# Optimization experiments

Measured on AMD Instinct MI355X. Metric: run time of the kernel, lower is better.

The kernel has to match this reference:

```python
import jax, jax.numpy as jnp
import numpy as np
from jax import lax

WIN = 5
EPS = 1e-08
SHAPE = (2, 1, 160, 192, 224)


def _box1d(x, axis, win):
    """Sliding-window sum of size `win` along `axis`, zero-padded (same size).
    Uses a cumsum difference -> O(1) work per voxel instead of dense conv."""
    pad = win // 2
    pw = [(0, 0)] * x.ndim
    pw[axis] = (pad + 1, pad)
    c = jnp.cumsum(jnp.pad(x, pw), axis=axis)
    n = x.shape[axis]
    hi = lax.slice_in_dim(c, win, win + n, axis=axis)
    lo = lax.slice_in_dim(c, 0, n, axis=axis)
    return hi - lo


def _box_sum3d(x, win):
    for axis in (2, 3, 4):
        x = _box1d(x, axis, win)
    return x


def setup_inputs() -> dict:
    key = jax.random.key(0)
    k1, k2, k3 = jax.random.split(key, 3)
    I = jax.random.uniform(k1, SHAPE, dtype=jnp.float32)
    J = jax.random.uniform(k2, SHAPE, dtype=jnp.float32)
    weight_map = jax.random.uniform(k3, SHAPE, dtype=jnp.float32)
    return {"I": I, "J": J, "weight_map": weight_map}


def reference(I, J, weight_map):
    win = WIN
    win_size = float(win ** 3)
    I_sum = _box_sum3d(I, win)
    J_sum = _box_sum3d(J, win)
    I2_sum = _box_sum3d(I * I, win)
    J2_sum = _box_sum3d(J * J, win)
    IJ_sum = _box_sum3d(I * J, win)
    u_I = I_sum / win_size
    u_J = J_sum / win_size
    cross = IJ_sum - u_J * I_sum - u_I * J_sum + u_I * u_J * win_size
    I_var = I2_sum - 2.0 * u_I * I_sum + u_I * u_I * win_size
    J_var = J2_sum - 2.0 * u_J * J_sum + u_J * u_J * win_size
    cc = cross * cross / (I_var * J_var + EPS)
    return -1.0 * jnp.mean(cc * weight_map)
```

## Files before the change

### kernel.cpp

```cpp
#include <hip/hip_runtime.h>

#define N_  2
#define D_  160
#define H_  192
#define W_  224
#define TW  32
#define TH  16
#define ZCH 20
#define NZC (D_/ZCH)
#define HR  (TH+4)
#define HC  (TW+4)
#define PL  (H_*W_)
#define TOT (N_*D_*H_*W_)

#define BAR() asm volatile("s_waitcnt lgkmcnt(0)\n\ts_barrier" ::: "memory")

__global__ __launch_bounds__(256, 4) void ncc_kernel(
    const float* __restrict__ I, const float* __restrict__ J,
    const float* __restrict__ Wm, float* __restrict__ out)
{
    __shared__ __align__(16) float zsL[5][HR][HC];
    __shared__ __align__(16) float sx [5][HR][HC];
    __shared__ float red[4];

    const int tid = threadIdx.x;
    const int bx = blockIdx.x, by = blockIdx.y;
    const int n  = blockIdx.z / NZC;
    const int c0 = (blockIdx.z % NZC) * ZCH;
    const int nbase = n * D_ * PL;

    const bool aAct = tid < 180;
    const int arow = tid / 9;
    const int ag   = tid % 9;
    const int ah   = by * TH - 2 + arow;
    const int ahc  = min(max(ah, 0), H_ - 1);
    const int aw0  = bx * TW - 2 + 4 * ag;
    const bool mH  = (ah == ahc);
    const bool mW0 = (aw0 >= 0);
    const bool mW1 = (aw0 + 3 < W_);
    const int awc0 = max(aw0, 0);
    const int awc1 = min(aw0 + 2, W_ - 4);
    const int preA0 = nbase + ahc * W_ + awc0;
    const int preA1 = nbase + ahc * W_ + awc1;

    const bool bAct = tid < 160;
    const int brow = tid >> 3;
    const int bxo  = (tid & 7) * 4;

    const int cty = tid >> 4;
    const int cx0 = (tid & 15) * 2;
    const int ch  = by * TH + cty;
    const int cw  = bx * TW + cx0;
    const int preW = nbase + ch * W_ + cw;

    float rI[4][5], rJ[4][5], zs[5][4];
#pragma unroll
    for (int c = 0; c < 4; ++c)
#pragma unroll
        for (int k = 0; k < 5; ++k) { rI[c][k] = 0.f; rJ[c][k] = 0.f; }
#pragma unroll
    for (int a = 0; a < 5; ++a)
#pragma unroll
        for (int c = 0; c < 4; ++c) zs[a][c] = 0.f;

    float acc = 0.f;
    const float inv125 = 1.0f / 125.0f;

    float cI[4] = {0.f,0.f,0.f,0.f}, cJ[4] = {0.f,0.f,0.f,0.f};
    {
        const int z0 = c0 - 2;
        const int zc = min(max(z0, 0), D_ - 1);
        const bool mZ = (z0 == zc);
        const int zoff = zc * PL;
        if (aAct) {
            const float2 i0 = *(const float2*)&I[preA0 + zoff];
            const float2 i1 = *(const float2*)&I[preA1 + zoff];
            const float2 j0 = *(const float2*)&J[preA0 + zoff];
            const float2 j1 = *(const float2*)&J[preA1 + zoff];
            const float f0 = (mH && mW0 && mZ) ? 1.f : 0.f;
            const float f1 = (mH && mW1 && mZ) ? 1.f : 0.f;
            cI[0]=i0.x*f0; cI[1]=i0.y*f0; cI[2]=i1.x*f1; cI[3]=i1.y*f1;
            cJ[0]=j0.x*f0; cJ[1]=j0.y*f0; cJ[2]=j1.x*f1; cJ[3]=j1.y*f1;
        }
    }
    float wmCx = 0.f, wmCy = 0.f;

    for (int s = 0; s < ZCH + 4; ++s) {
        const int zn  = c0 - 1 + s;
        const int znc = min(max(zn, 0), D_ - 1);
        const bool mZn = (zn == znc);
        const int zoffn = znc * PL;
        float2 pi0, pi1, pj0, pj1;
        if (aAct) {
            pi0 = *(const float2*)&I[preA0 + zoffn];
            pi1 = *(const float2*)&I[preA1 + zoffn];
            pj0 = *(const float2*)&J[preA0 + zoffn];
            pj1 = *(const float2*)&J[preA1 + zoffn];
        } else {
            pi0 = pi1 = pj0 = pj1 = make_float2(0.f, 0.f);
        }
        const int zon  = c0 - 3 + s;
        const int zonc = min(max(zon, 0), D_ - 1);
        const float2 wmN = *(const float2*)&Wm[preW + zonc * PL];

        if (aAct) {
#pragma unroll
            for (int c = 0; c < 4; ++c) {
                const float vi = cI[c], vj = cJ[c];
                const float oi = rI[c][0], oj = rJ[c][0];
                zs[0][c] += vi - oi;
                zs[1][c] += vj - oj;
                zs[2][c] += vi*vi - oi*oi;
                zs[3][c] += vj*vj - oj*oj;
                zs[4][c] += vi*vj - oi*oj;
#pragma unroll
                for (int k = 0; k < 4; ++k) { rI[c][k]=rI[c][k+1]; rJ[c][k]=rJ[c][k+1]; }
                rI[c][4] = vi; rJ[c][4] = vj;
            }
#pragma unroll
            for (int a = 0; a < 5; ++a)
                *(float4*)&zsL[a][arow][4*ag] =
                    make_float4(zs[a][0], zs[a][1], zs[a][2], zs[a][3]);
        }
        BAR();

        if (bAct) {
#pragma unroll
            for (int a = 0; a < 5; ++a) {
                const float4 v0 = *(const float4*)&zsL[a][brow][bxo];
                const float4 v1 = *(const float4*)&zsL[a][brow][bxo + 4];
                const float m  = v0.y + v0.z + v0.w;
                const float u1 = v1.x + v1.y;
                const float u2 = u1 + v1.z;
                *(float4*)&sx[a][brow][bxo] =
                    make_float4(v0.x + m + v1.x, m + u1,
                                (v0.z + v0.w) + u2, v0.w + (u2 + v1.w));
            }
        }
        BAR();

        if (s >= 4) {
            float2 S[5];
#pragma unroll
            for (int a = 0; a < 5; ++a) {
                float2 v = *(const float2*)&sx[a][cty][cx0];
#pragma unroll
                for (int k = 1; k < 5; ++k) {
                    const float2 w = *(const float2*)&sx[a][cty + k][cx0];
                    v.x += w.x; v.y += w.y;
                }
                S[a] = v;
            }
            {
                const float cr = S[4].x - S[0].x * S[1].x * inv125;
                const float vi = S[2].x - S[0].x * S[0].x * inv125;
                const float vj = S[3].x - S[1].x * S[1].x * inv125;
                acc += wmCx * (cr * cr) * __builtin_amdgcn_rcpf(vi * vj + 1e-8f);
            }
            {
                const float cr = S[4].y - S[0].y * S[1].y * inv125;
                const float vi = S[2].y - S[0].y * S[0].y * inv125;
                const float vj = S[3].y - S[1].y * S[1].y * inv125;
                acc += wmCy * (cr * cr) * __builtin_amdgcn_rcpf(vi * vj + 1e-8f);
            }
        }

        {
            const float f0 = (mH && mW0 && mZn) ? 1.f : 0.f;
            const float f1 = (mH && mW1 && mZn) ? 1.f : 0.f;
            cI[0]=pi0.x*f0; cI[1]=pi0.y*f0; cI[2]=pi1.x*f1; cI[3]=pi1.y*f1;
            cJ[0]=pj0.x*f0; cJ[1]=pj0.y*f0; cJ[2]=pj1.x*f1; cJ[3]=pj1.y*f1;
        }
        wmCx = wmN.x; wmCy = wmN.y;
    }

#pragma unroll
    for (int off = 32; off > 0; off >>= 1)
        acc += __shfl_down(acc, off, 64);
    const int wave = tid >> 6;
    const int lane = tid & 63;
    if (lane == 0) red[wave] = acc;
    __syncthreads();
    if (tid == 0) {
        const float t = red[0] + red[1] + red[2] + red[3];
        atomicAdd(out, t * (-1.0f / (float)TOT));
    }
}

extern "C" void kernel_launch(void* const* d_in, const int* in_sizes, int n_in,
                              void* d_out, int out_size, void* d_ws, size_t ws_size,
                              hipStream_t stream)
{
    const float* I  = (const float*)d_in[0];
    const float* J  = (const float*)d_in[1];
    const float* Wm = (const float*)d_in[2];
    float* out = (float*)d_out;

    hipMemsetAsync(out, 0, sizeof(float), stream);

    dim3 grid(W_ / TW, H_ / TH, N_ * NZC);
    dim3 block(256);
    hipLaunchKernelGGL(ncc_kernel, grid, block, 0, stream, I, J, Wm, out);
}
```

Measured before the change: 199.8 us.

## Enlarge tile height to 24 rows and use sliding-column y-sums per thread

After: 197.9 us. About the same (-0.9%).

```diff
diff --git a/kernel.cpp b/kernel.cpp
--- a/kernel.cpp
+++ b/kernel.cpp
@@ -5,7 +5,7 @@
 #define H_  192
 #define W_  224
 #define TW  32
-#define TH  16
+#define TH  24
 #define ZCH 20
 #define NZC (D_/ZCH)
 #define HR  (TH+4)
@@ -29,7 +29,7 @@
     const int c0 = (blockIdx.z % NZC) * ZCH;
     const int nbase = n * D_ * PL;
 
-    const bool aAct = tid < 180;
+    const bool aAct = tid < 252;
     const int arow = tid / 9;
     const int ag   = tid % 9;
     const int ah   = by * TH - 2 + arow;
@@ -43,15 +43,16 @@
     const int preA0 = nbase + ahc * W_ + awc0;
     const int preA1 = nbase + ahc * W_ + awc1;
 
-    const bool bAct = tid < 160;
+    const bool bAct = tid < 224;
     const int brow = tid >> 3;
     const int bxo  = (tid & 7) * 4;
 
-    const int cty = tid >> 4;
-    const int cx0 = (tid & 15) * 2;
-    const int ch  = by * TH + cty;
-    const int cw  = bx * TW + cx0;
-    const int preW = nbase + ch * W_ + cw;
+    const int cg   = tid >> 5;
+    const int cr0  = 3 * cg;
+    const int ccol = tid & 31;
+    const int ch0  = by * TH + cr0;
+    const int cw   = bx * TW + ccol;
+    const int preW = nbase + ch0 * W_ + cw;
 
     float rI[4][5], rJ[4][5], zs[5][4];
 #pragma unroll
@@ -83,7 +84,7 @@
             cJ[0]=j0.x*f0; cJ[1]=j0.y*f0; cJ[2]=j1.x*f1; cJ[3]=j1.y*f1;
         }
     }
-    float wmCx = 0.f, wmCy = 0.f;
+    float wm0 = 0.f, wm1 = 0.f, wm2 = 0.f;
 
     for (int s = 0; s < ZCH + 4; ++s) {
         const int zn  = c0 - 1 + s;
@@ -101,7 +102,10 @@
         }
         const int zon  = c0 - 3 + s;
         const int zonc = min(max(zon, 0), D_ - 1);
-        const float2 wmN = *(const float2*)&Wm[preW + zonc * PL];
+        const int wmo  = preW + zonc * PL;
+        const float wn0 = Wm[wmo];
+        const float wn1 = Wm[wmo + W_];
+        const float wn2 = Wm[wmo + 2 * W_];
 
         if (aAct) {
 #pragma unroll
@@ -140,28 +144,39 @@
         BAR();
 
         if (s >= 4) {
-            float2 S[5];
+            float S0[5], S1[5], S2[5];
 #pragma unroll
             for (int a = 0; a < 5; ++a) {
-                float2 v = *(const float2*)&sx[a][cty][cx0];
-#pragma unroll
-                for (int k = 1; k < 5; ++k) {
-                    const float2 w = *(const float2*)&sx[a][cty + k][cx0];
-                    v.x += w.x; v.y += w.y;
-                }
-                S[a] = v;
+                const float r0 = sx[a][cr0    ][ccol];
+                const float r1 = sx[a][cr0 + 1][ccol];
+                const float r2 = sx[a][cr0 + 2][ccol];
+                const float r3 = sx[a][cr0 + 3][ccol];
+                const float r4 = sx[a][cr0 + 4][ccol];
+                const float r5 = sx[a][cr0 + 5][ccol];
+                const float r6 = sx[a][cr0 + 6][ccol];
+                const float t0 = ((r0 + r1) + (r2 + r3)) + r4;
+                S0[a] = t0;
+                const float t1 = t0 - r0 + r5;
+                S1[a] = t1;
+                S2[a] = t1 - r1 + r6;
             }
             {
-                const float cr = S[4].x - S[0].x * S[1].x * inv125;
-                const float vi = S[2].x - S[0].x * S[0].x * inv125;
-                const float vj = S[3].x - S[1].x * S[1].x * inv125;
-                acc += wmCx * (cr * cr) * __builtin_amdgcn_rcpf(vi * vj + 1e-8f);
+                const float cr = S0[4] - S0[0] * S0[1] * inv125;
+                const float vi = S0[2] - S0[0] * S0[0] * inv125;
+                const float vj = S0[3] - S0[1] * S0[1] * inv125;
+                acc += wm0 * (cr * cr) * __builtin_amdgcn_rcpf(vi * vj + 1e-8f);
             }
             {
-                const float cr = S[4].y - S[0].y * S[1].y * inv125;
-                const float vi = S[2].y - S[0].y * S[0].y * inv125;
-                const float vj = S[3].y - S[1].y * S[1].y * inv125;
-                acc += wmCy * (cr * cr) * __builtin_amdgcn_rcpf(vi * vj + 1e-8f);
+                const float cr = S1[4] - S1[0] * S1[1] * inv125;
+                const float vi = S1[2] - S1[0] * S1[0] * inv125;
+                const float vj = S1[3] - S1[1] * S1[1] * inv125;
+                acc += wm1 * (cr * cr) * __builtin_amdgcn_rcpf(vi * vj + 1e-8f);
+            }
+            {
+                const float cr = S2[4] - S2[0] * S2[1] * inv125;
+                const float vi = S2[2] - S2[0] * S2[0] * inv125;
+                const float vj = S2[3] - S2[1] * S2[1] * inv125;
+                acc += wm2 * (cr * cr) * __builtin_amdgcn_rcpf(vi * vj + 1e-8f);
             }
         }
 
@@ -171,7 +186,7 @@
             cI[0]=pi0.x*f0; cI[1]=pi0.y*f0; cI[2]=pi1.x*f1; cI[3]=pi1.y*f1;
             cJ[0]=pj0.x*f0; cJ[1]=pj0.y*f0; cJ[2]=pj1.x*f1; cJ[3]=pj1.y*f1;
         }
-        wmCx = wmN.x; wmCy = wmN.y;
+        wm0 = wn0; wm1 = wn1; wm2 = wn2;
     }
 
 #pragma unroll
```
